# Optimization experiments

Measured on AMD Instinct MI355X. Metric: run time of the kernel, lower is better.

The kernel has to match this reference:

```python
import jax, jax.numpy as jnp
import numpy as np


def setup_inputs() -> dict:
    key = jax.random.key(0)
    kx, kc = jax.random.split(key)
    N, K, D = 32768, 4096, 512
    x = jax.random.normal(kx, (N, D), dtype=jnp.float32)
    # matches torch.rand(K, D) * 0.2 - 0.1
    codebook = jax.random.uniform(kc, (K, D), dtype=jnp.float32) * 0.2 - 0.1
    return {"x": x, "codebook": codebook}


def reference(x, codebook):
    x_sq = jnp.sum(x * x, axis=-1, keepdims=True)            # [N, 1]
    c_sq = jnp.sum(codebook * codebook, axis=-1)             # [K]
    dists = x_sq - 2.0 * jnp.einsum('nd,kd->nk', x, codebook) + c_sq[None, :]
    Z = jnp.argmin(dists, axis=-1)                           # [N] int
    q = codebook[Z]                                          # [N, D] gather
    q_with_st = x + jax.lax.stop_gradient(q - x)             # straight-through
    vq_loss = jnp.mean((jax.lax.stop_gradient(q) - x) ** 2)
    commitment_loss = jnp.mean((jax.lax.stop_gradient(x) - q) ** 2)
    return Z, q_with_st, vq_loss, commitment_loss
```

## Files before the change

### kernel.cpp

```cpp
#include <hip/hip_runtime.h>

static constexpr int N = 32768;
static constexpr int K = 4096;
static constexpr int D = 512;

typedef _Float16 f16x8 __attribute__((ext_vector_type(8)));
typedef float f32x4 __attribute__((ext_vector_type(4)));

#define GLD16(GP, LP)                                                   \
  __builtin_amdgcn_global_load_lds(                                     \
      (const __attribute__((address_space(1))) void*)(GP),              \
      (__attribute__((address_space(3))) void*)(LP), 16, 0, 0)

__global__ __launch_bounds__(256) void preprocess_kernel(
    const float* __restrict__ x, const float* __restrict__ cb,
    float* __restrict__ xsq, float* __restrict__ csq,
    _Float16* __restrict__ xhi, _Float16* __restrict__ chi,
    float* __restrict__ cbT) {
  __shared__ __align__(16) char lsraw[8 * 4 * 132 * 4];
  int bid = blockIdx.x;
  int tid = threadIdx.x;

  if (bid < 4096 + 512) {
    float (*ls)[4][132] = (float(*)[4][132])lsraw;
    const float* in;
    float* sqout;
    _Float16* hi;
    float scale;
    int rb;
    if (bid < 4096) {
      in = x; sqout = xsq; hi = xhi; scale = 16.0f; rb = bid * 8;
    } else {
      in = cb; sqout = csq; hi = chi; scale = 256.0f; rb = (bid - 4096) * 8;
    }
#pragma unroll
    for (int g2 = 0; g2 < 2; ++g2) {
      int g = g2 * 256 + tid;
      int r = g >> 6;
      int c8 = (g & 63) * 8;
      const float4* p = (const float4*)(in + (size_t)(rb + r) * D + c8);
      float4 a = p[0], b = p[1];
      float s[8] = {a.x, a.y, a.z, a.w, b.x, b.y, b.z, b.w};
      union { _Float16 h[8]; f16x8 v; } H;
      int blk = c8 >> 7, col = c8 & 127;
#pragma unroll
      for (int jj = 0; jj < 8; ++jj) {
        H.h[jj] = (_Float16)(s[jj] * scale);
        ls[r][blk][col + jj] = s[jj];
      }
      *(f16x8*)(hi + (size_t)(rb + r) * D + c8) = H.v;
    }
    __syncthreads();
    int rr = tid >> 5;
    int l = tid & 31;
    const float* p = &ls[rr][l >> 3][l & 7];
    float r = 0.f;
#pragma unroll
    for (int i = 0; i < 16; ++i) {
      float v = p[i * 8];
      r = __fadd_rn(r, __fmul_rn(v, v));
    }
    r = __fadd_rn(r, __shfl_xor(r, 1));
    r = __fadd_rn(r, __shfl_xor(r, 2));
    r = __fadd_rn(r, __shfl_xor(r, 4));
    r = __fadd_rn(r, __shfl_xor(r, 8));
    r = __fadd_rn(r, __shfl_xor(r, 16));
    if (l == 0) sqout[rb + rr] = r;
  } else {
    float (*t)[33] = (float(*)[33])lsraw;
    int tb = bid - 4608;
    int bk = tb >> 4;
    int bd = tb & 15;
    int tx = tid & 31, ty = tid >> 5;
#pragma unroll
    for (int j = 0; j < 32; j += 8)
      t[ty + j][tx] = cb[(size_t)(bk * 32 + ty + j) * D + bd * 32 + tx];
    __syncthreads();
#pragma unroll
    for (int j = 0; j < 32; j += 8)
      cbT[(size_t)(bd * 32 + ty + j) * K + bk * 32 + tx] = t[tx][ty + j];
  }
}

__global__ __launch_bounds__(256) void mfma_argmin_kernel(
    const _Float16* __restrict__ xh, const _Float16* __restrict__ ch,
    const float* __restrict__ xsq, const float* __restrict__ csq,
    float* __restrict__ pv1, int* __restrict__ pi1, float* __restrict__ pv2) {
  __shared__ __align__(16) _Float16 Ah[2][128 * 32];
  __shared__ __align__(16) _Float16 Bh[2][128 * 32];
  __shared__ float mbv1[128];
  __shared__ int mbi1[128];
  __shared__ float mbv2[128];

  int bid = blockIdx.x;
  int xcd = bid & 7, j = bid >> 3;
  int sup = j >> 6, win = j & 63;
  int rowPanel = xcd * 32 + (sup >> 2) * 8 + (win >> 3);
  int colPanel = (sup & 3) * 8 + (win & 7);

  int tid = threadIdx.x;
  int w = tid >> 6, l = tid & 63;
  int wr = w >> 1, wc = w & 1;
  int wrow = wr * 64, wcol = wc * 64;
  int rA = l & 15, g = l >> 4;

  const size_t rowBase = (size_t)rowPanel * 128;
  const size_t colBase = (size_t)colPanel * 128;

  f32x4 acc[4][4];
#pragma unroll
  for (int mi = 0; mi < 4; ++mi)
#pragma unroll
    for (int ni = 0; ni < 4; ++ni) acc[mi][ni] = (f32x4)0.f;

  const int r0 = tid >> 2, s0 = tid & 3;
  const int cs = s0 ^ ((r0 >> 1) & 3);
  const int swz = (g ^ ((rA >> 1) & 3)) * 8;

  const _Float16* aSrc = xh + (rowBase + r0) * D + cs * 8;
  const _Float16* bSrc = ch + (colBase + r0) * D + cs * 8;

  auto stage = [&](int buf, int kt) {
    const int dOff = kt * 32;
    GLD16(aSrc + dOff, &Ah[buf][(size_t)tid * 8]);
    GLD16(aSrc + dOff + (size_t)64 * D, &Ah[buf][(size_t)(tid + 256) * 8]);
    GLD16(bSrc + dOff, &Bh[buf][(size_t)tid * 8]);
    GLD16(bSrc + dOff + (size_t)64 * D, &Bh[buf][(size_t)(tid + 256) * 8]);
  };

  stage(0, 0);
  int cur = 0;
  for (int kt = 0; kt < 16; ++kt) {
    __syncthreads();
    if (kt < 15) stage(cur ^ 1, kt + 1);

    f16x8 ah[4], bh[4];
#pragma unroll
    for (int f = 0; f < 4; ++f) {
      ah[f] = *(const f16x8*)&Ah[cur][(wrow + f * 16 + rA) * 32 + swz];
      bh[f] = *(const f16x8*)&Bh[cur][(wcol + f * 16 + rA) * 32 + swz];
    }
#pragma unroll
    for (int mi = 0; mi < 4; ++mi)
#pragma unroll
      for (int ni = 0; ni < 4; ++ni)
        acc[mi][ni] =
            __builtin_amdgcn_mfma_f32_16x16x32_f16(ah[mi], bh[ni], acc[mi][ni], 0, 0, 0);
    cur ^= 1;
  }

  const float inv2048 = 1.0f / 2048.0f;
  float fv1[4][4], fv2[4][4];
  int fi1[4][4];
#pragma unroll
  for (int mi = 0; mi < 4; ++mi) {
#pragma unroll
    for (int r = 0; r < 4; ++r) {
      int row_l = wrow + mi * 16 + g * 4 + r;
      float xq = xsq[rowBase + row_l];
      float bv1 = 1e30f, bv2 = 1e30f;
      int bi1 = 0x7fffffff;
#pragma unroll
      for (int ni = 0; ni < 4; ++ni) {
        int col = (int)colBase + wcol + ni * 16 + rA;
        float S = acc[mi][ni][r];
        float dsc = (xq - S * inv2048) + csq[col];
        if (dsc < bv1 || (dsc == bv1 && col < bi1)) {
          bv2 = bv1; bv1 = dsc; bi1 = col;
        } else if (dsc < bv2) {
          bv2 = dsc;
        }
      }
#pragma unroll
      for (int m = 1; m < 16; m <<= 1) {
        float ov1 = __shfl_xor(bv1, m);
        int oi1 = __shfl_xor(bi1, m);
        float ov2 = __shfl_xor(bv2, m);
        if (ov1 < bv1 || (ov1 == bv1 && oi1 < bi1)) {
          bv2 = fminf(bv1, ov2); bv1 = ov1; bi1 = oi1;
        } else {
          bv2 = fminf(bv2, ov1);
        }
      }
      fv1[mi][r] = bv1; fv2[mi][r] = bv2; fi1[mi][r] = bi1;
      if (wc == 1 && rA == 0) {
        mbv1[row_l] = bv1; mbi1[row_l] = bi1; mbv2[row_l] = bv2;
      }
    }
  }
  __syncthreads();
  if (wc == 0 && rA == 0) {
#pragma unroll
    for (int mi = 0; mi < 4; ++mi) {
#pragma unroll
      for (int r = 0; r < 4; ++r) {
        int row_l = wrow + mi * 16 + g * 4 + r;
        float bv1 = fv1[mi][r], bv2 = fv2[mi][r];
        int bi1 = fi1[mi][r];
        float ov1 = mbv1[row_l];
        int oi1 = mbi1[row_l];
        float ov2 = mbv2[row_l];
        if (ov1 < bv1 || (ov1 == bv1 && oi1 < bi1)) {
          bv2 = fminf(bv1, ov2); bv1 = ov1; bi1 = oi1;
        } else {
          bv2 = fminf(bv2, ov1);
        }
        size_t o = (size_t)colPanel * N + (rowBase + row_l);
        pv1[o] = bv1; pi1[o] = bi1; pv2[o] = bv2;
      }
    }
  }
}

__global__ __launch_bounds__(256) void reduce_kernel(
    const float* __restrict__ pv1, const int* __restrict__ pi1,
    const float* __restrict__ pv2, float* __restrict__ zout,
    int* __restrict__ ctr, int* __restrict__ list, float eps) {
  int row = blockIdx.x * 256 + threadIdx.x;
  if (row >= N) return;
  float v1 = 1e30f, v2 = 1e30f;
  int i1 = 0x7fffffff;
  for (int jj = 0; jj < 32; ++jj) {
    float ov1 = pv1[(size_t)jj * N + row];
    float ov2 = pv2[(size_t)jj * N + row];
    int oi1 = pi1[(size_t)jj * N + row];
    if (ov1 < v1 || (ov1 == v1 && oi1 < i1)) {
      v2 = fminf(v1, ov2); v1 = ov1; i1 = oi1;
    } else {
      v2 = fminf(v2, ov1);
    }
  }
  zout[row] = (float)i1;
  if (v2 - v1 < eps) {
    int p = atomicAdd(ctr, 1);
    if (p < N) list[p] = row;
  }
}

static constexpr int RT_ROWS = 16;
static constexpr int RT_PANELS = 8;
static constexpr int CHUNK_D = 8;

__global__ __launch_bounds__(256) void rescore_tiled_kernel(
    const float* __restrict__ x, const float* __restrict__ cbT,
    const float* __restrict__ xsq, const float* __restrict__ csq,
    const int* __restrict__ ctr, const int* __restrict__ list,
    float* __restrict__ prv, int* __restrict__ pri) {
  __shared__ float xs[RT_ROWS][D + 4];
  __shared__ __align__(16) float cbs[2][CHUNK_D][512];
  int cnt = *ctr;
  if (cnt > N) cnt = N;
  int nTiles = (cnt + RT_ROWS - 1) / RT_ROWS;
  int nItems = nTiles * RT_PANELS;
  int tid = threadIdx.x;
  int ty = tid >> 4;
  int tx = tid & 15;

  for (int item = blockIdx.x; item < nItems; item += gridDim.x) {
    int tileIdx = item >> 3;
    int panel = item & 7;
    int base = tileIdx * RT_ROWS;
    int colPanel = panel * 512;
    __syncthreads();

    for (int i = tid; i < RT_ROWS * (D / 4); i += 256) {
      int r = i >> 7;
      int d4 = i & 127;
      int fi = base + r;
      int row = list[fi < cnt ? fi : 0];
      ((float4*)&xs[r][0])[d4] = ((const float4*)(x + (size_t)row * D))[d4];
    }

    auto stageCb = [&](int buf, int chk) {
      const float* src = cbT + (size_t)(chk * CHUNK_D) * K + colPanel;
#pragma unroll
      for (int it = 0; it < 4; ++it) {
        int f = it * 256 + tid;
        int dd = f >> 7, c4 = f & 127;
        GLD16(src + (size_t)dd * K + c4 * 4, &cbs[buf][0][0] + (size_t)f * 4);
      }
    };

    stageCb(0, 0);
    float acc[32];
#pragma unroll
    for (int c = 0; c < 32; ++c) acc[c] = 0.f;

    int cur = 0;
    for (int chk = 0; chk < D / CHUNK_D; ++chk) {
      __syncthreads();
      if (chk < D / CHUNK_D - 1) stageCb(cur ^ 1, chk + 1);
#pragma unroll
      for (int dd = 0; dd < CHUNK_D; ++dd) {
        float xa = xs[ty][chk * CHUNK_D + dd];
        const float4* cp = (const float4*)&cbs[cur][dd][0];
#pragma unroll
        for (int jj = 0; jj < 8; ++jj) {
          float4 v = cp[tx + jj * 16];
          acc[jj * 4 + 0] = fmaf(xa, v.x, acc[jj * 4 + 0]);
          acc[jj * 4 + 1] = fmaf(xa, v.y, acc[jj * 4 + 1]);
          acc[jj * 4 + 2] = fmaf(xa, v.z, acc[jj * 4 + 2]);
          acc[jj * 4 + 3] = fmaf(xa, v.w, acc[jj * 4 + 3]);
        }
      }
      cur ^= 1;
    }

    int fi = base + ty;
    int row = list[fi < cnt ? fi : 0];
    float xq = xsq[row];
    float bv = 1e30f;
    int bi = 0x7fffffff;
#pragma unroll
    for (int jj = 0; jj < 8; ++jj) {
#pragma unroll
      for (int q = 0; q < 4; ++q) {
        int col = colPanel + jj * 64 + tx * 4 + q;
        float a = acc[jj * 4 + q];
        float two = __fadd_rn(a, a);
        float t = __fsub_rn(xq, two);
        float dsc = __fadd_rn(t, csq[col]);
        if (dsc < bv || (dsc == bv && col < bi)) { bv = dsc; bi = col; }
      }
    }
#pragma unroll
    for (int m = 1; m < 16; m <<= 1) {
      float ov = __shfl_xor(bv, m);
      int oi = __shfl_xor(bi, m);
      if (ov < bv || (ov == bv && oi < bi)) { bv = ov; bi = oi; }
    }
    if (tx == 0 && fi < cnt) {
      prv[(size_t)fi * RT_PANELS + panel] = bv;
      pri[(size_t)fi * RT_PANELS + panel] = bi;
    }
  }
}

__global__ __launch_bounds__(256) void rescore_reduce_kernel(
    const float* __restrict__ prv, const int* __restrict__ pri,
    const int* __restrict__ ctr, const int* __restrict__ list,
    float* __restrict__ zout) {
  int cnt = *ctr;
  if (cnt > N) cnt = N;
  for (int fi = blockIdx.x * 256 + threadIdx.x; fi < cnt;
       fi += gridDim.x * 256) {
    float bv = 1e30f;
    int bi = 0x7fffffff;
#pragma unroll
    for (int p = 0; p < RT_PANELS; ++p) {
      float v = prv[(size_t)fi * RT_PANELS + p];
      int i = pri[(size_t)fi * RT_PANELS + p];
      if (v < bv || (v == bv && i < bi)) { bv = v; bi = i; }
    }
    zout[list[fi]] = (float)bi;
  }
}

static constexpr int BM = 64;
static constexpr int BKc = 128;
static constexpr int BD = 32;

__global__ __launch_bounds__(256) void argmin_fp32_kernel(
    const float* __restrict__ x, const float* __restrict__ cb,
    const float* __restrict__ xsq, const float* __restrict__ csq,
    float* __restrict__ zout) {
  __shared__ float xs[BD][BM];
  __shared__ float cs_[BD][BKc];
  __shared__ float mv[BM][16];
  __shared__ int mi[BM][16];

  int tid = threadIdx.x;
  int tx = tid & 15;
  int ty = tid >> 4;
  int row0 = blockIdx.x * BM;

  float bestv[4];
  int besti[4];
  float xsqr[4];
#pragma unroll
  for (int i = 0; i < 4; ++i) {
    bestv[i] = 3.4e38f;
    besti[i] = 0x7fffffff;
    xsqr[i] = xsq[row0 + ty * 4 + i];
  }

  for (int kt = 0; kt < K; kt += BKc) {
    float acc[4][8];
#pragma unroll
    for (int i = 0; i < 4; ++i)
#pragma unroll
      for (int jj = 0; jj < 8; ++jj) acc[i][jj] = 0.f;

    for (int dt = 0; dt < D; dt += BD) {
      __syncthreads();
      {
        int r = tid >> 2, d0 = (tid & 3) * 8;
        const float* src = x + (size_t)(row0 + r) * D + dt + d0;
        float4 v0 = *(const float4*)(src);
        float4 v1 = *(const float4*)(src + 4);
        xs[d0 + 0][r] = v0.x; xs[d0 + 1][r] = v0.y;
        xs[d0 + 2][r] = v0.z; xs[d0 + 3][r] = v0.w;
        xs[d0 + 4][r] = v1.x; xs[d0 + 5][r] = v1.y;
        xs[d0 + 6][r] = v1.z; xs[d0 + 7][r] = v1.w;
      }
      {
        int kk = tid >> 1, d0 = (tid & 1) * 16;
        const float* src = cb + (size_t)(kt + kk) * D + dt + d0;
        float4 v0 = *(const float4*)(src);
        float4 v1 = *(const float4*)(src + 4);
        float4 v2 = *(const float4*)(src + 8);
        float4 v3 = *(const float4*)(src + 12);
        cs_[d0 + 0][kk] = v0.x;  cs_[d0 + 1][kk] = v0.y;
        cs_[d0 + 2][kk] = v0.z;  cs_[d0 + 3][kk] = v0.w;
        cs_[d0 + 4][kk] = v1.x;  cs_[d0 + 5][kk] = v1.y;
        cs_[d0 + 6][kk] = v1.z;  cs_[d0 + 7][kk] = v1.w;
        cs_[d0 + 8][kk] = v2.x;  cs_[d0 + 9][kk] = v2.y;
        cs_[d0 + 10][kk] = v2.z; cs_[d0 + 11][kk] = v2.w;
        cs_[d0 + 12][kk] = v3.x; cs_[d0 + 13][kk] = v3.y;
        cs_[d0 + 14][kk] = v3.z; cs_[d0 + 15][kk] = v3.w;
      }
      __syncthreads();
#pragma unroll 4
      for (int d = 0; d < BD; ++d) {
        float xa[4], cv[8];
        *(float4*)&xa[0] = *(const float4*)&xs[d][ty * 4];
        *(float4*)&cv[0] = *(const float4*)&cs_[d][tx * 8];
        *(float4*)&cv[4] = *(const float4*)&cs_[d][tx * 8 + 4];
#pragma unroll
        for (int i = 0; i < 4; ++i)
#pragma unroll
          for (int jj = 0; jj < 8; ++jj)
            acc[i][jj] = fmaf(xa[i], cv[jj], acc[i][jj]);
      }
    }

#pragma unroll
    for (int jj = 0; jj < 8; ++jj) {
      int k = kt + tx * 8 + jj;
      float cq = csq[k];
#pragma unroll
      for (int i = 0; i < 4; ++i) {
        float two = __fadd_rn(acc[i][jj], acc[i][jj]);
        float t = __fsub_rn(xsqr[i], two);
        float dsc = __fadd_rn(t, cq);
        if (dsc < bestv[i]) { bestv[i] = dsc; besti[i] = k; }
      }
    }
  }

  __syncthreads();
#pragma unroll
  for (int i = 0; i < 4; ++i) {
    mv[ty * 4 + i][tx] = bestv[i];
    mi[ty * 4 + i][tx] = besti[i];
  }
  __syncthreads();
  if (tid < BM) {
    float bv = mv[tid][0];
    int bi = mi[tid][0];
#pragma unroll
    for (int t = 1; t < 16; ++t) {
      float v = mv[tid][t];
      int ii = mi[tid][t];
      if (v < bv || (v == bv && ii < bi)) { bv = v; bi = ii; }
    }
    zout[row0 + tid] = (float)bi;
  }
}

__global__ __launch_bounds__(256) void gather_kernel(
    const float* __restrict__ x, const float* __restrict__ cb,
    const float* __restrict__ zf, float* __restrict__ qout,
    float* __restrict__ partial) {
  __shared__ float red[256];
  const size_t TOT4 = (size_t)N * D / 4;
  size_t t0 = (size_t)blockIdx.x * 256 + threadIdx.x;
  float lsum = 0.f;
  for (size_t f = t0; f < TOT4; f += (size_t)2048 * 256) {
    int n = (int)(f >> 7);
    int d4 = (int)(f & 127);
    int z = (int)zf[n];
    float4 xv = ((const float4*)x)[f];
    float4 qv = *(const float4*)(cb + (size_t)z * D + d4 * 4);
    float dx0 = __fsub_rn(qv.x, xv.x);
    float dx1 = __fsub_rn(qv.y, xv.y);
    float dx2 = __fsub_rn(qv.z, xv.z);
    float dx3 = __fsub_rn(qv.w, xv.w);
    float4 o;
    o.x = __fadd_rn(xv.x, dx0);
    o.y = __fadd_rn(xv.y, dx1);
    o.z = __fadd_rn(xv.z, dx2);
    o.w = __fadd_rn(xv.w, dx3);
    ((float4*)qout)[f] = o;
    lsum += dx0 * dx0 + dx1 * dx1 + dx2 * dx2 + dx3 * dx3;
  }
  red[threadIdx.x] = lsum;
  __syncthreads();
  for (int s = 128; s > 0; s >>= 1) {
    if (threadIdx.x < s) red[threadIdx.x] += red[threadIdx.x + s];
    __syncthreads();
  }
  if (threadIdx.x == 0) partial[blockIdx.x] = red[0];
}

__global__ __launch_bounds__(256) void loss_kernel(const float* __restrict__ partial,
                                                   float* __restrict__ loss_out) {
  __shared__ float red[256];
  float s = 0.f;
  for (int i = threadIdx.x; i < 2048; i += 256) s += partial[i];
  red[threadIdx.x] = s;
  __syncthreads();
  for (int k = 128; k > 0; k >>= 1) {
    if (threadIdx.x < k) red[threadIdx.x] += red[threadIdx.x + k];
    __syncthreads();
  }
  if (threadIdx.x == 0) {
    float m = red[0] / (float)((size_t)N * D);
    loss_out[0] = m;
    loss_out[1] = m;
  }
}

static constexpr size_t OFF_XSQ = 0;
static constexpr size_t OFF_CSQ = 131072;
static constexpr size_t OFF_PART = 147456;
static constexpr size_t OFF_CTR = 155648;
static constexpr size_t OFF_LIST = 155904;
static constexpr size_t OFF_PV1 = 286976;
static constexpr size_t OFF_PI1 = OFF_PV1 + 4194304;
static constexpr size_t OFF_PV2 = OFF_PI1 + 4194304;
static constexpr size_t OFF_PRV = OFF_PV2 + 4194304;
static constexpr size_t OFF_PRI = OFF_PRV + 1048576;
static constexpr size_t WS_REQ = OFF_PRI + 1048576;

extern "C" void kernel_launch(void* const* d_in, const int* in_sizes, int n_in,
                              void* d_out, int out_size, void* d_ws, size_t ws_size,
                              hipStream_t stream) {
  const float* x = (const float*)d_in[0];
  const float* cb = (const float*)d_in[1];
  float* out = (float*)d_out;

  float* zout = out;
  float* qout = out + N;
  float* lout = out + N + (size_t)N * D;

  char* ws = (char*)d_ws;
  float* xsq = (float*)(ws + OFF_XSQ);
  float* csq = (float*)(ws + OFF_CSQ);
  float* partial = (float*)(ws + OFF_PART);

  _Float16* xhi = (_Float16*)qout;
  float* cbT = (float*)((char*)qout + (size_t)N * D * 2);
  _Float16* chi = (_Float16*)((char*)cbT + (size_t)D * K * 4);

  if (ws_size >= WS_REQ) {
    int* ctr = (int*)(ws + OFF_CTR);
    int* list = (int*)(ws + OFF_LIST);
    float* pv1 = (float*)(ws + OFF_PV1);
    int* pi1 = (int*)(ws + OFF_PI1);
    float* pv2 = (float*)(ws + OFF_PV2);
    float* prv = (float*)(ws + OFF_PRV);
    int* pri = (int*)(ws + OFF_PRI);

    preprocess_kernel<<<dim3(4096 + 512 + 2048), dim3(256), 0, stream>>>(
        x, cb, xsq, csq, xhi, chi, cbT);
    hipMemsetAsync(ctr, 0, sizeof(int), stream);
    mfma_argmin_kernel<<<dim3((N / 128) * (K / 128)), dim3(256), 0, stream>>>(
        xhi, chi, xsq, csq, pv1, pi1, pv2);
    reduce_kernel<<<dim3(N / 256), dim3(256), 0, stream>>>(pv1, pi1, pv2, zout,
                                                           ctr, list, 0.02f);
    rescore_tiled_kernel<<<dim3(1024), dim3(256), 0, stream>>>(
        x, cbT, xsq, csq, ctr, list, prv, pri);
    rescore_reduce_kernel<<<dim3(128), dim3(256), 0, stream>>>(prv, pri, ctr,
                                                               list, zout);
  } else {
    preprocess_kernel<<<dim3(4096 + 512 + 2048), dim3(256), 0, stream>>>(
        x, cb, xsq, csq, xhi, chi, cbT);
    argmin_fp32_kernel<<<dim3(N / BM), dim3(256), 0, stream>>>(x, cb, xsq, csq,
                                                               zout);
  }

  gather_kernel<<<dim3(2048), dim3(256), 0, stream>>>(x, cb, zout, qout, partial);
  loss_kernel<<<dim3(1), dim3(256), 0, stream>>>(partial, lout);
}
```

Measured before the change: 532.0 us.

## Process two column panels per argmin block and widen gather with nontemporal stores

Each MFMA argmin block now handles two adjacent 128-column codebook panels in sequence. The first k-tile of the next panel is prefetched during the last iteration of the current one, and the grid is halved. This amortises block launch and prologue cost, but the A tile is reloaded per panel, so it adds little data reuse. The gather kernel doubles its grid and uses nontemporal stores for the q output, the loss reduction is resized to match, and the workspace offsets shift to fit the larger partial buffer.

```diff
diff --git a/kernel.cpp b/kernel.cpp
--- a/kernel.cpp
+++ b/kernel.cpp
@@ -95,8 +95,8 @@
   int bid = blockIdx.x;
   int xcd = bid & 7, j = bid >> 3;
   int sup = j >> 6, win = j & 63;
-  int rowPanel = xcd * 32 + (sup >> 2) * 8 + (win >> 3);
-  int colPanel = (sup & 3) * 8 + (win & 7);
+  int rowPanel = xcd * 32 + (sup >> 1) * 8 + (win >> 3);
+  int colPanelBase = ((sup & 1) * 8 + (win & 7)) * 2;
 
   int tid = threadIdx.x;
   int w = tid >> 6, l = tid & 63;
@@ -105,108 +105,117 @@
   int rA = l & 15, g = l >> 4;
 
   const size_t rowBase = (size_t)rowPanel * 128;
-  const size_t colBase = (size_t)colPanel * 128;
-
-  f32x4 acc[4][4];
-#pragma unroll
-  for (int mi = 0; mi < 4; ++mi)
-#pragma unroll
-    for (int ni = 0; ni < 4; ++ni) acc[mi][ni] = (f32x4)0.f;
 
   const int r0 = tid >> 2, s0 = tid & 3;
   const int cs = s0 ^ ((r0 >> 1) & 3);
   const int swz = (g ^ ((rA >> 1) & 3)) * 8;
 
   const _Float16* aSrc = xh + (rowBase + r0) * D + cs * 8;
-  const _Float16* bSrc = ch + (colBase + r0) * D + cs * 8;
-
-  auto stage = [&](int buf, int kt) {
+
+  auto stage = [&](int buf, int colPanel, int kt) {
     const int dOff = kt * 32;
+    const _Float16* bS = ch + ((size_t)colPanel * 128 + r0) * D + cs * 8;
     GLD16(aSrc + dOff, &Ah[buf][(size_t)tid * 8]);
     GLD16(aSrc + dOff + (size_t)64 * D, &Ah[buf][(size_t)(tid + 256) * 8]);
-    GLD16(bSrc + dOff, &Bh[buf][(size_t)tid * 8]);
-    GLD16(bSrc + dOff + (size_t)64 * D, &Bh[buf][(size_t)(tid + 256) * 8]);
+    GLD16(bS + dOff, &Bh[buf][(size_t)tid * 8]);
+    GLD16(bS + dOff + (size_t)64 * D, &Bh[buf][(size_t)(tid + 256) * 8]);
   };
 
-  stage(0, 0);
+  stage(0, colPanelBase, 0);
   int cur = 0;
-  for (int kt = 0; kt < 16; ++kt) {
-    __syncthreads();
-    if (kt < 15) stage(cur ^ 1, kt + 1);
-
-    f16x8 ah[4], bh[4];
-#pragma unroll
-    for (int f = 0; f < 4; ++f) {
-      ah[f] = *(const f16x8*)&Ah[cur][(wrow + f * 16 + rA) * 32 + swz];
-      bh[f] = *(const f16x8*)&Bh[cur][(wcol + f * 16 + rA) * 32 + swz];
-    }
+
+  for (int pp = 0; pp < 2; ++pp) {
+    const int colPanel = colPanelBase + pp;
+    const size_t colBase = (size_t)colPanel * 128;
+
+    f32x4 acc[4][4];
 #pragma unroll
     for (int mi = 0; mi < 4; ++mi)
 #pragma unroll
-      for (int ni = 0; ni < 4; ++ni)
-        acc[mi][ni] =
-            __builtin_amdgcn_mfma_f32_16x16x32_f16(ah[mi], bh[ni], acc[mi][ni], 0, 0, 0);
-    cur ^= 1;
-  }
-
-  const float inv2048 = 1.0f / 2048.0f;
-  float fv1[4][4], fv2[4][4];
-  int fi1[4][4];
-#pragma unroll
-  for (int mi = 0; mi < 4; ++mi) {
-#pragma unroll
-    for (int r = 0; r < 4; ++r) {
-      int row_l = wrow + mi * 16 + g * 4 + r;
-      float xq = xsq[rowBase + row_l];
-      float bv1 = 1e30f, bv2 = 1e30f;
-      int bi1 = 0x7fffffff;
-#pragma unroll
-      for (int ni = 0; ni < 4; ++ni) {
-        int col = (int)colBase + wcol + ni * 16 + rA;
-        float S = acc[mi][ni][r];
-        float dsc = (xq - S * inv2048) + csq[col];
-        if (dsc < bv1 || (dsc == bv1 && col < bi1)) {
-          bv2 = bv1; bv1 = dsc; bi1 = col;
-        } else if (dsc < bv2) {
-          bv2 = dsc;
-        }
-      }
-#pragma unroll
-      for (int m = 1; m < 16; m <<= 1) {
-        float ov1 = __shfl_xor(bv1, m);
-        int oi1 = __shfl_xor(bi1, m);
-        float ov2 = __shfl_xor(bv2, m);
-        if (ov1 < bv1 || (ov1 == bv1 && oi1 < bi1)) {
-          bv2 = fminf(bv1, ov2); bv1 = ov1; bi1 = oi1;
-        } else {
-          bv2 = fminf(bv2, ov1);
-        }
-      }
-      fv1[mi][r] = bv1; fv2[mi][r] = bv2; fi1[mi][r] = bi1;
-      if (wc == 1 && rA == 0) {
-        mbv1[row_l] = bv1; mbi1[row_l] = bi1; mbv2[row_l] = bv2;
-      }
-    }
-  }
-  __syncthreads();
-  if (wc == 0 && rA == 0) {
+      for (int ni = 0; ni < 4; ++ni) acc[mi][ni] = (f32x4)0.f;
+
+    for (int kt = 0; kt < 16; ++kt) {
+      __syncthreads();
+      if (kt < 15) {
+        stage(cur ^ 1, colPanel, kt + 1);
+      } else if (pp == 0) {
+        stage(cur ^ 1, colPanel + 1, 0);
+      }
+
+      f16x8 ah[4], bh[4];
+#pragma unroll
+      for (int f = 0; f < 4; ++f) {
+        ah[f] = *(const f16x8*)&Ah[cur][(wrow + f * 16 + rA) * 32 + swz];
+        bh[f] = *(const f16x8*)&Bh[cur][(wcol + f * 16 + rA) * 32 + swz];
+      }
+#pragma unroll
+      for (int mi = 0; mi < 4; ++mi)
+#pragma unroll
+        for (int ni = 0; ni < 4; ++ni)
+          acc[mi][ni] =
+              __builtin_amdgcn_mfma_f32_16x16x32_f16(ah[mi], bh[ni], acc[mi][ni], 0, 0, 0);
+      cur ^= 1;
+    }
+
+    const float inv2048 = 1.0f / 2048.0f;
+    float fv1[4][4], fv2[4][4];
+    int fi1[4][4];
 #pragma unroll
     for (int mi = 0; mi < 4; ++mi) {
 #pragma unroll
       for (int r = 0; r < 4; ++r) {
         int row_l = wrow + mi * 16 + g * 4 + r;
-        float bv1 = fv1[mi][r], bv2 = fv2[mi][r];
-        int bi1 = fi1[mi][r];
-        float ov1 = mbv1[row_l];
-        int oi1 = mbi1[row_l];
-        float ov2 = mbv2[row_l];
-        if (ov1 < bv1 || (ov1 == bv1 && oi1 < bi1)) {
-          bv2 = fminf(bv1, ov2); bv1 = ov1; bi1 = oi1;
-        } else {
-          bv2 = fminf(bv2, ov1);
+        float xq = xsq[rowBase + row_l];
+        float bv1 = 1e30f, bv2 = 1e30f;
+        int bi1 = 0x7fffffff;
+#pragma unroll
+        for (int ni = 0; ni < 4; ++ni) {
+          int col = (int)colBase + wcol + ni * 16 + rA;
+          float S = acc[mi][ni][r];
+          float dsc = (xq - S * inv2048) + csq[col];
+          if (dsc < bv1 || (dsc == bv1 && col < bi1)) {
+            bv2 = bv1; bv1 = dsc; bi1 = col;
+          } else if (dsc < bv2) {
+            bv2 = dsc;
+          }
         }
-        size_t o = (size_t)colPanel * N + (rowBase + row_l);
-        pv1[o] = bv1; pi1[o] = bi1; pv2[o] = bv2;
+#pragma unroll
+        for (int m = 1; m < 16; m <<= 1) {
+          float ov1 = __shfl_xor(bv1, m);
+          int oi1 = __shfl_xor(bi1, m);
+          float ov2 = __shfl_xor(bv2, m);
+          if (ov1 < bv1 || (ov1 == bv1 && oi1 < bi1)) {
+            bv2 = fminf(bv1, ov2); bv1 = ov1; bi1 = oi1;
+          } else {
+            bv2 = fminf(bv2, ov1);
+          }
+        }
+        fv1[mi][r] = bv1; fv2[mi][r] = bv2; fi1[mi][r] = bi1;
+        if (wc == 1 && rA == 0) {
+          mbv1[row_l] = bv1; mbi1[row_l] = bi1; mbv2[row_l] = bv2;
+        }
+      }
+    }
+    __syncthreads();
+    if (wc == 0 && rA == 0) {
+#pragma unroll
+      for (int mi = 0; mi < 4; ++mi) {
+#pragma unroll
+        for (int r = 0; r < 4; ++r) {
+          int row_l = wrow + mi * 16 + g * 4 + r;
+          float bv1 = fv1[mi][r], bv2 = fv2[mi][r];
+          int bi1 = fi1[mi][r];
+          float ov1 = mbv1[row_l];
+          int oi1 = mbi1[row_l];
+          float ov2 = mbv2[row_l];
+          if (ov1 < bv1 || (ov1 == bv1 && oi1 < bi1)) {
+            bv2 = fminf(bv1, ov2); bv1 = ov1; bi1 = oi1;
+          } else {
+            bv2 = fminf(bv2, ov1);
+          }
+          size_t o = (size_t)colPanel * N + (rowBase + row_l);
+          pv1[o] = bv1; pi1[o] = bi1; pv2[o] = bv2;
+        }
       }
     }
   }
@@ -476,7 +485,7 @@
   const size_t TOT4 = (size_t)N * D / 4;
   size_t t0 = (size_t)blockIdx.x * 256 + threadIdx.x;
   float lsum = 0.f;
-  for (size_t f = t0; f < TOT4; f += (size_t)2048 * 256) {
+  for (size_t f = t0; f < TOT4; f += (size_t)4096 * 256) {
     int n = (int)(f >> 7);
     int d4 = (int)(f & 127);
     int z = (int)zf[n];
@@ -486,12 +495,12 @@
     float dx1 = __fsub_rn(qv.y, xv.y);
     float dx2 = __fsub_rn(qv.z, xv.z);
     float dx3 = __fsub_rn(qv.w, xv.w);
-    float4 o;
-    o.x = __fadd_rn(xv.x, dx0);
-    o.y = __fadd_rn(xv.y, dx1);
-    o.z = __fadd_rn(xv.z, dx2);
-    o.w = __fadd_rn(xv.w, dx3);
-    ((float4*)qout)[f] = o;
+    f32x4 o;
+    o[0] = __fadd_rn(xv.x, dx0);
+    o[1] = __fadd_rn(xv.y, dx1);
+    o[2] = __fadd_rn(xv.z, dx2);
+    o[3] = __fadd_rn(xv.w, dx3);
+    __builtin_nontemporal_store(o, (f32x4*)qout + f);
     lsum += dx0 * dx0 + dx1 * dx1 + dx2 * dx2 + dx3 * dx3;
   }
   red[threadIdx.x] = lsum;
@@ -507,7 +516,7 @@
                                                    float* __restrict__ loss_out) {
   __shared__ float red[256];
   float s = 0.f;
-  for (int i = threadIdx.x; i < 2048; i += 256) s += partial[i];
+  for (int i = threadIdx.x; i < 4096; i += 256) s += partial[i];
   red[threadIdx.x] = s;
   __syncthreads();
   for (int k = 128; k > 0; k >>= 1) {
@@ -524,9 +533,9 @@
 static constexpr size_t OFF_XSQ = 0;
 static constexpr size_t OFF_CSQ = 131072;
 static constexpr size_t OFF_PART = 147456;
-static constexpr size_t OFF_CTR = 155648;
-static constexpr size_t OFF_LIST = 155904;
-static constexpr size_t OFF_PV1 = 286976;
+static constexpr size_t OFF_CTR = 163840;
+static constexpr size_t OFF_LIST = 164096;
+static constexpr size_t OFF_PV1 = 295168;
 static constexpr size_t OFF_PI1 = OFF_PV1 + 4194304;
 static constexpr size_t OFF_PV2 = OFF_PI1 + 4194304;
 static constexpr size_t OFF_PRV = OFF_PV2 + 4194304;
@@ -565,7 +574,7 @@
     preprocess_kernel<<<dim3(4096 + 512 + 2048), dim3(256), 0, stream>>>(
         x, cb, xsq, csq, xhi, chi, cbT);
     hipMemsetAsync(ctr, 0, sizeof(int), stream);
-    mfma_argmin_kernel<<<dim3((N / 128) * (K / 128)), dim3(256), 0, stream>>>(
+    mfma_argmin_kernel<<<dim3((N / 128) * (K / 256)), dim3(256), 0, stream>>>(
         xhi, chi, xsq, csq, pv1, pi1, pv2);
     reduce_kernel<<<dim3(N / 256), dim3(256), 0, stream>>>(pv1, pi1, pv2, zout,
                                                            ctr, list, 0.02f);
@@ -580,6 +589,6 @@
                                                                zout);
   }
 
-  gather_kernel<<<dim3(2048), dim3(256), 0, stream>>>(x, cb, zout, qout, partial);
+  gather_kernel<<<dim3(4096), dim3(256), 0, stream>>>(x, cb, zout, qout, partial);
   loss_kernel<<<dim3(1), dim3(256), 0, stream>>>(partial, lout);
 }
```

Result: slower. 923.9 us (+73.7%).
